# Optimization experiments

Hardware: AMD Instinct MI355X
Metric: run time of the kernel (lower is better)

## Reference

```python
import jax, jax.numpy as jnp
import numpy as np

B, N, C, H = 8, 1024, 768, 12
D = C // H  # head_dim = 64
SCALE = D ** -0.5


def setup_inputs() -> dict:
    key = jax.random.key(0)
    ks = jax.random.split(key, 5)
    s = lambda k, sh, fan: jax.random.normal(k, sh, jnp.float32) * (fan ** -0.5)
    return {
        "x": jax.random.normal(ks[0], (B, N, C), jnp.float32),
        "w_qkv": s(ks[1], (C, 3 * C), C),
        "b_qkv": jnp.zeros((3 * C,), jnp.float32),
        "w_l": s(ks[2], (H, H), H),
        "b_l": jnp.zeros((H,), jnp.float32),
        "w_w": s(ks[3], (H, H), H),
        "b_w": jnp.zeros((H,), jnp.float32),
        "w_proj": s(ks[4], (C, C), C),
        "b_proj": jnp.zeros((C,), jnp.float32),
    }


def reference(x, w_qkv, b_qkv, w_l, b_l, w_w, b_w, w_proj, b_proj):
    Bq, Nq, Cq = x.shape
    # qkv projection -> (3, B, H, N, D)
    qkv = (x @ w_qkv + b_qkv).reshape(Bq, Nq, 3, H, D).transpose(2, 0, 3, 1, 4)
    q, k, v = qkv[0] * SCALE, qkv[1], qkv[2]
    # raw scores [B, H, N, N]
    attn = jnp.einsum("bhnd,bhmd->bhnm", q, k)
    # pre-softmax talking-heads: mix across head axis (Dense over H)
    attn = jnp.einsum("bhnm,hg->bgnm", attn, w_l) + b_l[None, :, None, None]
    attn = jax.nn.softmax(attn, axis=-1)
    # post-softmax talking-heads
    attn = jnp.einsum("bhnm,hg->bgnm", attn, w_w) + b_w[None, :, None, None]
    # weighted values -> (B, N, C)
    out = jnp.einsum("bhnm,bhmd->bnhd", attn, v).reshape(Bq, Nq, Cq)
    return out @ w_proj + b_proj
```

## Files before the change

### kernel.cpp

```cpp
#include <hip/hip_runtime.h>

#define BB 8
#define NN 1024
#define CC 768
#define HH 12
#define DD 64

typedef unsigned short u16;
typedef unsigned int u32;
typedef __attribute__((ext_vector_type(8))) short s16x8;
typedef __attribute__((ext_vector_type(4))) short s16x4;
typedef __attribute__((ext_vector_type(4))) float f32x4;
typedef __attribute__((ext_vector_type(4))) u32 u32x4;

__device__ __forceinline__ float bf2f(u16 u) {
  u32 x = ((u32)u) << 16;
  return __builtin_bit_cast(float, x);
}
__device__ __forceinline__ u16 f2bf(float f) {
  u32 x = __builtin_bit_cast(u32, f);
  x += 0x7fffu + ((x >> 16) & 1u);
  return (u16)(x >> 16);
}

__global__ __launch_bounds__(256) void convx_kernel(const float* __restrict__ in,
                                                    u16* __restrict__ out) {
  size_t i = ((size_t)blockIdx.x * 256 + threadIdx.x) * 8;
  f32x4 a = *(const f32x4*)(in + i);
  f32x4 b = *(const f32x4*)(in + i + 4);
  s16x8 r;
#pragma unroll
  for (int j = 0; j < 4; j++) { r[j] = (short)f2bf(a[j]); r[4 + j] = (short)f2bf(b[j]); }
  *(s16x8*)(out + i) = r;
}

__global__ __launch_bounds__(256) void transpose_kernel(const float* __restrict__ in,
                                                        u16* __restrict__ out,
                                                        int R, int C) {
  __shared__ float t[32][33];
  const int cl = threadIdx.x & 31, rq = threadIdx.x >> 5;
#pragma unroll
  for (int rr = 0; rr < 4; rr++) {
    int rl = rq * 4 + rr;
    t[rl][cl] = in[(size_t)(blockIdx.y * 32 + rl) * C + blockIdx.x * 32 + cl];
  }
  __syncthreads();
#pragma unroll
  for (int rr = 0; rr < 4; rr++) {
    int oc = rq * 4 + rr;
    out[(size_t)(blockIdx.x * 32 + oc) * R + blockIdx.y * 32 + cl] = f2bf(t[cl][oc]);
  }
}

__global__ __launch_bounds__(256) void qkv_gemm(
    const u16* __restrict__ A, const u16* __restrict__ Bt, const float* __restrict__ bias,
    u16* __restrict__ qo, u16* __restrict__ ko, u16* __restrict__ vo) {
  __shared__ __align__(16) u16 As[128 * 32];
  __shared__ __align__(16) u16 Bs[128 * 32];
  const int tid = threadIdx.x;
  const int w = tid >> 6, lane = tid & 63, l15 = lane & 15, l4 = lane >> 4;
  const int wm = w & 1, wn = w >> 1;
  const int m0 = blockIdx.x * 128, n0 = blockIdx.y * 128;
  const int sr = lane >> 2, sk = (lane & 3) * 8;

  f32x4 acc[4][4];
#pragma unroll
  for (int a = 0; a < 4; a++)
#pragma unroll
    for (int bb = 0; bb < 4; bb++) acc[a][bb] = (f32x4){0.f, 0.f, 0.f, 0.f};

  for (int k0 = 0; k0 < CC; k0 += 32) {
    s16x8 a0 = *(const s16x8*)(A + (size_t)(m0 + w * 16 + sr) * CC + k0 + sk);
    s16x8 a1 = *(const s16x8*)(A + (size_t)(m0 + 64 + w * 16 + sr) * CC + k0 + sk);
    s16x8 b0 = *(const s16x8*)(Bt + (size_t)(n0 + w * 16 + sr) * CC + k0 + sk);
    s16x8 b1 = *(const s16x8*)(Bt + (size_t)(n0 + 64 + w * 16 + sr) * CC + k0 + sk);
    __syncthreads();
    *(s16x8*)&As[(w * 16 + sr) * 32 + sk] = a0;
    *(s16x8*)&As[(64 + w * 16 + sr) * 32 + sk] = a1;
    *(s16x8*)&Bs[(w * 16 + sr) * 32 + sk] = b0;
    *(s16x8*)&Bs[(64 + w * 16 + sr) * 32 + sk] = b1;
    __syncthreads();
    s16x8 af[4], bf[4];
#pragma unroll
    for (int a = 0; a < 4; a++) af[a] = *(const s16x8*)&As[(wm * 64 + a * 16 + l15) * 32 + l4 * 8];
#pragma unroll
    for (int bb = 0; bb < 4; bb++) bf[bb] = *(const s16x8*)&Bs[(wn * 64 + bb * 16 + l15) * 32 + l4 * 8];
#pragma unroll
    for (int a = 0; a < 4; a++)
#pragma unroll
      for (int bb = 0; bb < 4; bb++)
        acc[a][bb] = __builtin_amdgcn_mfma_f32_16x16x32_bf16(af[a], bf[bb], acc[a][bb], 0, 0, 0);
  }

  const int b = (m0 >> 10);
#pragma unroll
  for (int bb = 0; bb < 4; bb++) {
    int col = n0 + wn * 64 + bb * 16 + l15;
    int s = col / CC;
    int rem = col - s * CC;
    int h = rem >> 6, d = rem & 63;
    float bv = bias[col];
#pragma unroll
    for (int a = 0; a < 4; a++) {
      int row0 = m0 + wm * 64 + a * 16 + l4 * 4;
      int nt0 = row0 & (NN - 1);
      if (s == 2) {
        s16x4 pk;
#pragma unroll
        for (int r = 0; r < 4; r++) pk[r] = (short)f2bf(acc[a][bb][r] + bv);
        *(s16x4*)(vo + (((size_t)((b * HH + h) * DD + d)) << 10) + nt0) = pk;
      } else if (s == 0) {
#pragma unroll
        for (int r = 0; r < 4; r++)
          qo[(((size_t)((b * HH + h) * NN + nt0 + r)) << 6) + d] = f2bf((acc[a][bb][r] + bv) * 0.125f);
      } else {
#pragma unroll
        for (int r = 0; r < 4; r++)
          ko[(((size_t)((b * HH + h) * NN + nt0 + r)) << 6) + d] = f2bf(acc[a][bb][r] + bv);
      }
    }
  }
}

__global__ __launch_bounds__(256) void proj_gemm(
    const u16* __restrict__ A, const u16* __restrict__ Bt, const float* __restrict__ bias,
    float* __restrict__ out) {
  __shared__ __align__(16) u16 As[128 * 32];
  __shared__ __align__(16) u16 Bs[128 * 32];
  const int tid = threadIdx.x;
  const int w = tid >> 6, lane = tid & 63, l15 = lane & 15, l4 = lane >> 4;
  const int wm = w & 1, wn = w >> 1;
  const int m0 = blockIdx.x * 128, n0 = blockIdx.y * 128;
  const int sr = lane >> 2, sk = (lane & 3) * 8;

  f32x4 acc[4][4];
#pragma unroll
  for (int a = 0; a < 4; a++)
#pragma unroll
    for (int bb = 0; bb < 4; bb++) acc[a][bb] = (f32x4){0.f, 0.f, 0.f, 0.f};

  for (int k0 = 0; k0 < CC; k0 += 32) {
    s16x8 a0 = *(const s16x8*)(A + (size_t)(m0 + w * 16 + sr) * CC + k0 + sk);
    s16x8 a1 = *(const s16x8*)(A + (size_t)(m0 + 64 + w * 16 + sr) * CC + k0 + sk);
    s16x8 b0 = *(const s16x8*)(Bt + (size_t)(n0 + w * 16 + sr) * CC + k0 + sk);
    s16x8 b1 = *(const s16x8*)(Bt + (size_t)(n0 + 64 + w * 16 + sr) * CC + k0 + sk);
    __syncthreads();
    *(s16x8*)&As[(w * 16 + sr) * 32 + sk] = a0;
    *(s16x8*)&As[(64 + w * 16 + sr) * 32 + sk] = a1;
    *(s16x8*)&Bs[(w * 16 + sr) * 32 + sk] = b0;
    *(s16x8*)&Bs[(64 + w * 16 + sr) * 32 + sk] = b1;
    __syncthreads();
    s16x8 af[4], bf[4];
#pragma unroll
    for (int a = 0; a < 4; a++) af[a] = *(const s16x8*)&As[(wm * 64 + a * 16 + l15) * 32 + l4 * 8];
#pragma unroll
    for (int bb = 0; bb < 4; bb++) bf[bb] = *(const s16x8*)&Bs[(wn * 64 + bb * 16 + l15) * 32 + l4 * 8];
#pragma unroll
    for (int a = 0; a < 4; a++)
#pragma unroll
      for (int bb = 0; bb < 4; bb++)
        acc[a][bb] = __builtin_amdgcn_mfma_f32_16x16x32_bf16(af[a], bf[bb], acc[a][bb], 0, 0, 0);
  }

#pragma unroll
  for (int bb = 0; bb < 4; bb++) {
    int col = n0 + wn * 64 + bb * 16 + l15;
    float bv = bias[col];
#pragma unroll
    for (int a = 0; a < 4; a++) {
      int row0 = m0 + wm * 64 + a * 16 + l4 * 4;
#pragma unroll
      for (int r = 0; r < 4; r++)
        out[(size_t)(row0 + r) * CC + col] = acc[a][bb][r] + bv;
    }
  }
}

#define SB_OFF 0
#define UT_OFF 24576
#define LINV_OFF 45056
#define LPART_OFF 46144
#define SM_TOTAL 54336

__global__ __launch_bounds__(512, 4) void attn_kernel(
    const u16* __restrict__ qg, const u16* __restrict__ kg, const u16* __restrict__ vtg,
    const float* __restrict__ wlg, const float* __restrict__ blg,
    const float* __restrict__ wwg, const float* __restrict__ bwg,
    u16* __restrict__ aout) {
  __shared__ __align__(16) char smem[SM_TOTAL];
  u16* Sb = (u16*)(smem + SB_OFF);
  u16* Ut = (u16*)(smem + UT_OFF);
  float* linv = (float*)(smem + LINV_OFF);
  float* lpart = (float*)(smem + LPART_OFF);

  const int b = blockIdx.x;
  const int i0 = blockIdx.y * 16;
  const int tid = threadIdx.x;
  const int w = tid >> 6, lane = tid & 63, l15 = lane & 15, l4 = lane >> 4;

  s16x8 wlA1, wlA2, wwA1, wwA2;
#pragma unroll
  for (int j = 0; j < 8; j++) {
    int k = l4 * 8 + j, hh = k >> 1, pt = k & 1, g = l15;
    float wlv = (hh < 12 && g < 12) ? wlg[hh * 12 + g] : 0.f;
    float wwv = (hh < 12 && g < 12) ? wwg[hh * 12 + g] : 0.f;
    u16 h1 = f2bf(wlv); u16 lo1 = f2bf(wlv - bf2f(h1));
    u16 h2 = f2bf(wwv); u16 lo2 = f2bf(wwv - bf2f(h2));
    wlA1[j] = (short)h1; wlA2[j] = (short)(pt ? 0 : lo1);
    wwA1[j] = (short)h2; wwA2[j] = (short)(pt ? 0 : lo2);
  }
  float blv[4], bwv[4];
#pragma unroll
  for (int r = 0; r < 4; r++) {
    int g = l4 * 4 + r;
    blv[r] = (g < 12) ? blg[g] : 0.f;
    bwv[r] = (g < 12) ? bwg[g] : 0.f;
  }

  int jh[3], jmb[3];
  s16x8 qf[3][2];
#pragma unroll
  for (int jt = 0; jt < 3; jt++) {
    int j = w * 3 + jt;
    jh[jt] = j % 12; jmb[jt] = j / 12;
    const u16* qp = qg + (((size_t)((b * HH + jh[jt]) * NN + i0 + l15)) << 6) + l4 * 8;
    qf[jt][0] = *(const s16x8*)(qp);
    qf[jt][1] = *(const s16x8*)(qp + 32);
  }

  float la[4] = {0.f, 0.f, 0.f, 0.f};
  for (int mt = 0; mt < NN / 32; mt++) {
    const int m0 = mt * 32;
#pragma unroll
    for (int jt = 0; jt < 3; jt++) {
      f32x4 c = (f32x4){0.f, 0.f, 0.f, 0.f};
      const u16* kp = kg + (((size_t)((b * HH + jh[jt]) * NN + m0 + jmb[jt] * 16 + l15)) << 6) + l4 * 8;
      s16x8 a0 = *(const s16x8*)(kp);
      s16x8 a1 = *(const s16x8*)(kp + 32);
      c = __builtin_amdgcn_mfma_f32_16x16x32_bf16(a0, qf[jt][0], c, 0, 0, 0);
      c = __builtin_amdgcn_mfma_f32_16x16x32_bf16(a1, qf[jt][1], c, 0, 0, 0);
      int cb = (jmb[jt] * 16 + l4 * 4) * 16 + l15;
#pragma unroll
      for (int r = 0; r < 4; r++) {
        float v = c[r];
        u16 hi = f2bf(v); u16 lo = f2bf(v - bf2f(hi));
        *(u32*)(Sb + (size_t)(cb + r * 16) * 24 + 2 * jh[jt]) = (u32)hi | ((u32)lo << 16);
      }
    }
    __syncthreads();
#pragma unroll
    for (int tt = 0; tt < 4; tt++) {
      int t = w * 4 + tt;
      s16x8 bS = *(const s16x8*)(Sb + (size_t)(t * 16 + l15) * 24 + l4 * 8);
      f32x4 T = (f32x4){blv[0], blv[1], blv[2], blv[3]};
      T = __builtin_amdgcn_mfma_f32_16x16x32_bf16(wlA1, bS, T, 0, 0, 0);
      T = __builtin_amdgcn_mfma_f32_16x16x32_bf16(wlA2, bS, T, 0, 0, 0);
#pragma unroll
      for (int r = 0; r < 4; r++) la[r] += __expf(T[r]);
    }
    __syncthreads();
  }

#pragma unroll
  for (int r = 0; r < 4; r++) lpart[w * 256 + (l4 * 4 + r) * 16 + l15] = la[r];
  __syncthreads();
  if (tid < 256) {
    float s = 0.f;
#pragma unroll
    for (int w2 = 0; w2 < 8; w2++) s += lpart[w2 * 256 + tid];
    linv[(tid >> 4) * 17 + (tid & 15)] = 1.f / s;
  }
  __syncthreads();
  float linv_l[4];
#pragma unroll
  for (int r = 0; r < 4; r++) linv_l[r] = linv[(l4 * 4 + r) * 17 + l15];

  const int db = w >> 1, pvh = (w & 1) * 6;
  f32x4 O[6];
#pragma unroll
  for (int jp = 0; jp < 6; jp++) O[jp] = (f32x4){0.f, 0.f, 0.f, 0.f};

  for (int mt = 0; mt < NN / 32; mt++) {
    const int m0 = mt * 32;
#pragma unroll
    for (int jt = 0; jt < 3; jt++) {
      f32x4 c = (f32x4){0.f, 0.f, 0.f, 0.f};
      const u16* kp = kg + (((size_t)((b * HH + jh[jt]) * NN + m0 + jmb[jt] * 16 + l15)) << 6) + l4 * 8;
      s16x8 a0 = *(const s16x8*)(kp);
      s16x8 a1 = *(const s16x8*)(kp + 32);
      c = __builtin_amdgcn_mfma_f32_16x16x32_bf16(a0, qf[jt][0], c, 0, 0, 0);
      c = __builtin_amdgcn_mfma_f32_16x16x32_bf16(a1, qf[jt][1], c, 0, 0, 0);
      int cb = (jmb[jt] * 16 + l4 * 4) * 16 + l15;
#pragma unroll
      for (int r = 0; r < 4; r++) {
        float v = c[r];
        u16 hi = f2bf(v); u16 lo = f2bf(v - bf2f(hi));
        *(u32*)(Sb + (size_t)(cb + r * 16) * 24 + 2 * jh[jt]) = (u32)hi | ((u32)lo << 16);
      }
    }
    __syncthreads();
#pragma unroll
    for (int tt = 0; tt < 4; tt++) {
      int t = w * 4 + tt;
      s16x8 bS = *(const s16x8*)(Sb + (size_t)(t * 16 + l15) * 24 + l4 * 8);
      f32x4 T = (f32x4){blv[0], blv[1], blv[2], blv[3]};
      T = __builtin_amdgcn_mfma_f32_16x16x32_bf16(wlA1, bS, T, 0, 0, 0);
      T = __builtin_amdgcn_mfma_f32_16x16x32_bf16(wlA2, bS, T, 0, 0, 0);
      u32x4 pk;
#pragma unroll
      for (int r = 0; r < 4; r++) {
        float P = __expf(T[r]) * linv_l[r];
        u16 hi = f2bf(P); u16 lo = f2bf(P - bf2f(hi));
        pk[r] = (u32)hi | ((u32)lo << 16);
      }
      s16x8 bP = __builtin_bit_cast(s16x8, pk);
      f32x4 U = (f32x4){bwv[0], bwv[1], bwv[2], bwv[3]};
      U = __builtin_amdgcn_mfma_f32_16x16x32_bf16(wwA1, bP, U, 0, 0, 0);
      U = __builtin_amdgcn_mfma_f32_16x16x32_bf16(wwA2, bP, U, 0, 0, 0);
#pragma unroll
      for (int r = 0; r < 4; r++)
        Ut[(size_t)((l4 * 4 + r) * 16 + l15) * 40 + t] = f2bf(U[r]);
    }
    __syncthreads();
#pragma unroll
    for (int jp = 0; jp < 6; jp++) {
      const int h = pvh + jp;
      s16x8 aV = *(const s16x8*)(vtg + (((size_t)((b * HH + h) * DD + db * 16 + l15)) << 10) + m0 + l4 * 8);
      s16x8 bU = *(const s16x8*)(Ut + (size_t)(h * 16 + l15) * 40 + l4 * 8);
      O[jp] = __builtin_amdgcn_mfma_f32_16x16x32_bf16(aV, bU, O[jp], 0, 0, 0);
    }
    __syncthreads();
  }

#pragma unroll
  for (int jp = 0; jp < 6; jp++) {
    const int h = pvh + jp;
    const int d0 = db * 16 + l4 * 4;
    s16x4 pk4;
#pragma unroll
    for (int r = 0; r < 4; r++) pk4[r] = (short)f2bf(O[jp][r]);
    *(s16x4*)(aout + ((size_t)(b * NN) + i0 + l15) * CC + h * DD + d0) = pk4;
  }
}

extern "C" void kernel_launch(void* const* d_in, const int* in_sizes, int n_in,
                              void* d_out, int out_size, void* d_ws, size_t ws_size,
                              hipStream_t stream) {
  const float* x      = (const float*)d_in[0];
  const float* w_qkv  = (const float*)d_in[1];
  const float* b_qkv  = (const float*)d_in[2];
  const float* w_l    = (const float*)d_in[3];
  const float* b_l    = (const float*)d_in[4];
  const float* w_w    = (const float*)d_in[5];
  const float* b_w    = (const float*)d_in[6];
  const float* w_proj = (const float*)d_in[7];
  const float* b_proj = (const float*)d_in[8];

  const size_t per = (size_t)BB * HH * NN * DD;
  u16* xb  = (u16*)d_ws;
  u16* wqt = xb + per;
  u16* wpt = wqt + (size_t)3 * CC * CC;
  u16* q   = wpt + (size_t)CC * CC;
  u16* k   = q + per;
  u16* vt  = k + per;
  u16* ao  = vt + per;

  convx_kernel<<<3072, 256, 0, stream>>>(x, xb);
  transpose_kernel<<<dim3(3 * CC / 32, CC / 32), 256, 0, stream>>>(w_qkv, wqt, CC, 3 * CC);
  transpose_kernel<<<dim3(CC / 32, CC / 32), 256, 0, stream>>>(w_proj, wpt, CC, CC);
  qkv_gemm<<<dim3(64, 18), 256, 0, stream>>>(xb, wqt, b_qkv, q, k, vt);
  attn_kernel<<<dim3(BB, NN / 16), 512, 0, stream>>>(q, k, vt, w_l, b_l, w_w, b_w, ao);
  proj_gemm<<<dim3(64, 6), 256, 0, stream>>>(ao, wpt, b_proj, (float*)d_out);
}
```

Before: 454.5 us.

## Fold softmax normalization into exp2 bias, single-bf16 pass one, double-buffer Ut

Scales the pre-softmax mixing weights and bias by 1/ln2 so hardware exp2 replaces expf. The row normalizer becomes a log2 subtracted in the MFMA accumulator init, which removes the per-element multiply. The first (sum) pass uses plain bf16 scores with one MFMA instead of hi/lo split, and hi-part extraction becomes truncation. Ut is double-buffered to drop one barrier per iteration, and the LDS strides are changed, with 8-byte reads used for the unaligned rows. The bf16-only first pass and truncated hi parts may shift accuracy slightly.

```diff
diff --git a/kernel.cpp b/kernel.cpp
--- a/kernel.cpp
+++ b/kernel.cpp
@@ -11,6 +11,7 @@
 typedef __attribute__((ext_vector_type(8))) short s16x8;
 typedef __attribute__((ext_vector_type(4))) short s16x4;
 typedef __attribute__((ext_vector_type(4))) float f32x4;
+typedef __attribute__((ext_vector_type(2))) u32 u32x2;
 typedef __attribute__((ext_vector_type(4))) u32 u32x4;
 
 __device__ __forceinline__ float bf2f(u16 u) {
@@ -21,6 +22,14 @@
   u32 x = __builtin_bit_cast(u32, f);
   x += 0x7fffu + ((x >> 16) & 1u);
   return (u16)(x >> 16);
+}
+__device__ __forceinline__ float hw_exp2(float x) { return __builtin_amdgcn_exp2f(x); }
+__device__ __forceinline__ float hw_log2(float x) { return __builtin_amdgcn_logf(x); }
+__device__ __forceinline__ s16x8 lds_read8(const u16* p) {
+  u32x2 a = *(const u32x2*)p;
+  u32x2 b = *(const u32x2*)(p + 4);
+  u32x4 m = {a.x, a.y, b.x, b.y};
+  return __builtin_bit_cast(s16x8, m);
 }
 
 __global__ __launch_bounds__(256) void convx_kernel(const float* __restrict__ in,
@@ -176,11 +185,11 @@
   }
 }
 
-#define SB_OFF 0
-#define UT_OFF 24576
-#define LINV_OFF 45056
-#define LPART_OFF 46144
-#define SM_TOTAL 54336
+#define SB_BYTES 28736
+#define UT_OFF   SB_BYTES
+#define UT_ELE   6912
+#define LL2_OFF  (SB_BYTES + 27648)
+#define SM_TOTAL (LL2_OFF + 1088)
 
 __global__ __launch_bounds__(512, 4) void attn_kernel(
     const u16* __restrict__ qg, const u16* __restrict__ kg, const u16* __restrict__ vtg,
@@ -188,33 +197,38 @@
     const float* __restrict__ wwg, const float* __restrict__ bwg,
     u16* __restrict__ aout) {
   __shared__ __align__(16) char smem[SM_TOTAL];
-  u16* Sb = (u16*)(smem + SB_OFF);
-  u16* Ut = (u16*)(smem + UT_OFF);
-  float* linv = (float*)(smem + LINV_OFF);
-  float* lpart = (float*)(smem + LPART_OFF);
-
-  const int b = blockIdx.x;
-  const int i0 = blockIdx.y * 16;
+  u16* Sb = (u16*)smem;
+  u16* Ut0 = (u16*)(smem + UT_OFF);
+  float* lpart = (float*)(smem + UT_OFF);
+  float* ll2 = (float*)(smem + LL2_OFF);
+
+  const int b = blockIdx.x, i0 = blockIdx.y * 16;
   const int tid = threadIdx.x;
   const int w = tid >> 6, lane = tid & 63, l15 = lane & 15, l4 = lane >> 4;
-
-  s16x8 wlA1, wlA2, wwA1, wwA2;
+  const float RLN2 = 1.44269504088896340736f;
+
+  for (int j = tid; j < SB_BYTES / 4; j += 512) ((u32*)smem)[j] = 0;
+
+  s16x8 wlS, wlA1, wlA2, wwA1, wwA2;
 #pragma unroll
   for (int j = 0; j < 8; j++) {
-    int k = l4 * 8 + j, hh = k >> 1, pt = k & 1, g = l15;
-    float wlv = (hh < 12 && g < 12) ? wlg[hh * 12 + g] : 0.f;
-    float wwv = (hh < 12 && g < 12) ? wwg[hh * 12 + g] : 0.f;
-    u16 h1 = f2bf(wlv); u16 lo1 = f2bf(wlv - bf2f(h1));
-    u16 h2 = f2bf(wwv); u16 lo2 = f2bf(wwv - bf2f(h2));
-    wlA1[j] = (short)h1; wlA2[j] = (short)(pt ? 0 : lo1);
-    wwA1[j] = (short)h2; wwA2[j] = (short)(pt ? 0 : lo2);
-  }
-  float blv[4], bwv[4];
+    int k = l4 * 8 + j;
+    float v1 = (k < 12 && l15 < 12) ? wlg[k * 12 + l15] * RLN2 : 0.f;
+    wlS[j] = (short)f2bf(v1);
+    int h = k >> 1, pt = k & 1;
+    float v2 = (h < 12 && l15 < 12) ? wlg[h * 12 + l15] * RLN2 : 0.f;
+    u16 h2 = f2bf(v2); u16 lo2 = f2bf(v2 - bf2f(h2));
+    wlA1[j] = (short)h2; wlA2[j] = (short)(pt ? 0 : lo2);
+    float v3 = (h < 12 && l15 < 12) ? wwg[h * 12 + l15] : 0.f;
+    u16 h3 = f2bf(v3); u16 lo3 = f2bf(v3 - bf2f(h3));
+    wwA1[j] = (short)h3; wwA2[j] = (short)(pt ? 0 : lo3);
+  }
+  int gr[4]; float blv[4], bwv[4];
 #pragma unroll
   for (int r = 0; r < 4; r++) {
-    int g = l4 * 4 + r;
-    blv[r] = (g < 12) ? blg[g] : 0.f;
-    bwv[r] = (g < 12) ? bwg[g] : 0.f;
+    gr[r] = l4 * 4 + r;
+    blv[r] = (gr[r] < 12) ? blg[gr[r]] * RLN2 : 0.f;
+    bwv[r] = (gr[r] < 12) ? bwg[gr[r]] : 0.f;
   }
 
   int jh[3], jmb[3];
@@ -224,94 +238,91 @@
     int j = w * 3 + jt;
     jh[jt] = j % 12; jmb[jt] = j / 12;
     const u16* qp = qg + (((size_t)((b * HH + jh[jt]) * NN + i0 + l15)) << 6) + l4 * 8;
-    qf[jt][0] = *(const s16x8*)(qp);
+    qf[jt][0] = *(const s16x8*)qp;
     qf[jt][1] = *(const s16x8*)(qp + 32);
   }
 
   float la[4] = {0.f, 0.f, 0.f, 0.f};
-  for (int mt = 0; mt < NN / 32; mt++) {
+  for (int mt = 0; mt < 32; mt++) {
     const int m0 = mt * 32;
 #pragma unroll
     for (int jt = 0; jt < 3; jt++) {
       f32x4 c = (f32x4){0.f, 0.f, 0.f, 0.f};
       const u16* kp = kg + (((size_t)((b * HH + jh[jt]) * NN + m0 + jmb[jt] * 16 + l15)) << 6) + l4 * 8;
-      s16x8 a0 = *(const s16x8*)(kp);
-      s16x8 a1 = *(const s16x8*)(kp + 32);
-      c = __builtin_amdgcn_mfma_f32_16x16x32_bf16(a0, qf[jt][0], c, 0, 0, 0);
-      c = __builtin_amdgcn_mfma_f32_16x16x32_bf16(a1, qf[jt][1], c, 0, 0, 0);
+      c = __builtin_amdgcn_mfma_f32_16x16x32_bf16(*(const s16x8*)kp, qf[jt][0], c, 0, 0, 0);
+      c = __builtin_amdgcn_mfma_f32_16x16x32_bf16(*(const s16x8*)(kp + 32), qf[jt][1], c, 0, 0, 0);
       int cb = (jmb[jt] * 16 + l4 * 4) * 16 + l15;
 #pragma unroll
-      for (int r = 0; r < 4; r++) {
-        float v = c[r];
-        u16 hi = f2bf(v); u16 lo = f2bf(v - bf2f(hi));
-        *(u32*)(Sb + (size_t)(cb + r * 16) * 24 + 2 * jh[jt]) = (u32)hi | ((u32)lo << 16);
-      }
+      for (int r = 0; r < 4; r++)
+        Sb[(size_t)(cb + r * 16) * 20 + jh[jt]] = f2bf(c[r]);
     }
     __syncthreads();
 #pragma unroll
     for (int tt = 0; tt < 4; tt++) {
       int t = w * 4 + tt;
-      s16x8 bS = *(const s16x8*)(Sb + (size_t)(t * 16 + l15) * 24 + l4 * 8);
+      s16x8 bS = lds_read8(Sb + (size_t)(t * 16 + l15) * 20 + l4 * 8);
       f32x4 T = (f32x4){blv[0], blv[1], blv[2], blv[3]};
-      T = __builtin_amdgcn_mfma_f32_16x16x32_bf16(wlA1, bS, T, 0, 0, 0);
-      T = __builtin_amdgcn_mfma_f32_16x16x32_bf16(wlA2, bS, T, 0, 0, 0);
-#pragma unroll
-      for (int r = 0; r < 4; r++) la[r] += __expf(T[r]);
-    }
-    __syncthreads();
-  }
-
-#pragma unroll
-  for (int r = 0; r < 4; r++) lpart[w * 256 + (l4 * 4 + r) * 16 + l15] = la[r];
+      T = __builtin_amdgcn_mfma_f32_16x16x32_bf16(wlS, bS, T, 0, 0, 0);
+#pragma unroll
+      for (int r = 0; r < 4; r++) la[r] += hw_exp2(T[r]);
+    }
+    __syncthreads();
+  }
+
+#pragma unroll
+  for (int r = 0; r < 4; r++) lpart[w * 256 + gr[r] * 16 + l15] = la[r];
   __syncthreads();
   if (tid < 256) {
     float s = 0.f;
 #pragma unroll
     for (int w2 = 0; w2 < 8; w2++) s += lpart[w2 * 256 + tid];
-    linv[(tid >> 4) * 17 + (tid & 15)] = 1.f / s;
+    ll2[(tid >> 4) * 17 + (tid & 15)] = hw_log2(s);
   }
   __syncthreads();
-  float linv_l[4];
-#pragma unroll
-  for (int r = 0; r < 4; r++) linv_l[r] = linv[(l4 * 4 + r) * 17 + l15];
+  float Tinit[4];
+#pragma unroll
+  for (int r = 0; r < 4; r++) Tinit[r] = blv[r] - ll2[gr[r] * 17 + l15];
 
   const int db = w >> 1, pvh = (w & 1) * 6;
   f32x4 O[6];
 #pragma unroll
   for (int jp = 0; jp < 6; jp++) O[jp] = (f32x4){0.f, 0.f, 0.f, 0.f};
 
-  for (int mt = 0; mt < NN / 32; mt++) {
+  for (int mt = 0; mt < 32; mt++) {
     const int m0 = mt * 32;
+    u16* Utb = Ut0 + (mt & 1) * UT_ELE;
 #pragma unroll
     for (int jt = 0; jt < 3; jt++) {
       f32x4 c = (f32x4){0.f, 0.f, 0.f, 0.f};
       const u16* kp = kg + (((size_t)((b * HH + jh[jt]) * NN + m0 + jmb[jt] * 16 + l15)) << 6) + l4 * 8;
-      s16x8 a0 = *(const s16x8*)(kp);
-      s16x8 a1 = *(const s16x8*)(kp + 32);
-      c = __builtin_amdgcn_mfma_f32_16x16x32_bf16(a0, qf[jt][0], c, 0, 0, 0);
-      c = __builtin_amdgcn_mfma_f32_16x16x32_bf16(a1, qf[jt][1], c, 0, 0, 0);
+      c = __builtin_amdgcn_mfma_f32_16x16x32_bf16(*(const s16x8*)kp, qf[jt][0], c, 0, 0, 0);
+      c = __builtin_amdgcn_mfma_f32_16x16x32_bf16(*(const s16x8*)(kp + 32), qf[jt][1], c, 0, 0, 0);
       int cb = (jmb[jt] * 16 + l4 * 4) * 16 + l15;
 #pragma unroll
       for (int r = 0; r < 4; r++) {
         float v = c[r];
-        u16 hi = f2bf(v); u16 lo = f2bf(v - bf2f(hi));
-        *(u32*)(Sb + (size_t)(cb + r * 16) * 24 + 2 * jh[jt]) = (u32)hi | ((u32)lo << 16);
+        u32 xv = __builtin_bit_cast(u32, v);
+        float hf = __builtin_bit_cast(float, xv & 0xFFFF0000u);
+        u16 lo = f2bf(v - hf);
+        *(u32*)(Sb + (size_t)(cb + r * 16) * 28 + 2 * jh[jt]) = (xv >> 16) | ((u32)lo << 16);
       }
     }
     __syncthreads();
 #pragma unroll
     for (int tt = 0; tt < 4; tt++) {
       int t = w * 4 + tt;
-      s16x8 bS = *(const s16x8*)(Sb + (size_t)(t * 16 + l15) * 24 + l4 * 8);
-      f32x4 T = (f32x4){blv[0], blv[1], blv[2], blv[3]};
+      s16x8 bS = lds_read8(Sb + (size_t)(t * 16 + l15) * 28 + l4 * 8);
+      f32x4 T = (f32x4){Tinit[0], Tinit[1], Tinit[2], Tinit[3]};
       T = __builtin_amdgcn_mfma_f32_16x16x32_bf16(wlA1, bS, T, 0, 0, 0);
       T = __builtin_amdgcn_mfma_f32_16x16x32_bf16(wlA2, bS, T, 0, 0, 0);
       u32x4 pk;
 #pragma unroll
       for (int r = 0; r < 4; r++) {
-        float P = __expf(T[r]) * linv_l[r];
-        u16 hi = f2bf(P); u16 lo = f2bf(P - bf2f(hi));
-        pk[r] = (u32)hi | ((u32)lo << 16);
+        float P = hw_exp2(T[r]);
+        u32 xp = __builtin_bit_cast(u32, P);
+        float hf = __builtin_bit_cast(float, xp & 0xFFFF0000u);
+        u16 lo = f2bf(P - hf);
+        pk[r] = (xp >> 16) | ((u32)lo << 16);
       }
       s16x8 bP = __builtin_bit_cast(s16x8, pk);
       f32x4 U = (f32x4){bwv[0], bwv[1], bwv[2], bwv[3]};
@@ -319,17 +330,16 @@
       U = __builtin_amdgcn_mfma_f32_16x16x32_bf16(wwA2, bP, U, 0, 0, 0);
 #pragma unroll
       for (int r = 0; r < 4; r++)
-        Ut[(size_t)((l4 * 4 + r) * 16 + l15) * 40 + t] = f2bf(U[r]);
+        if (gr[r] < 12) Utb[(size_t)(gr[r] * 16 + l15) * 36 + t] = f2bf(U[r]);
     }
     __syncthreads();
 #pragma unroll
     for (int jp = 0; jp < 6; jp++) {
       const int h = pvh + jp;
       s16x8 aV = *(const s16x8*)(vtg + (((size_t)((b * HH + h) * DD + db * 16 + l15)) << 10) + m0 + l4 * 8);
-      s16x8 bU = *(const s16x8*)(Ut + (size_t)(h * 16 + l15) * 40 + l4 * 8);
+      s16x8 bU = lds_read8(Utb + (size_t)(h * 16 + l15) * 36 + l4 * 8);
       O[jp] = __builtin_amdgcn_mfma_f32_16x16x32_bf16(aV, bU, O[jp], 0, 0, 0);
     }
-    __syncthreads();
   }
 
 #pragma unroll
```

Result: no change. 448.1 us (-1.4%).
